# Kernel optimization log

Measured on AMD Instinct MI355X. Metric: run time of the kernel, lower is better.

Reference implementation:

```python
import jax, jax.numpy as jnp
import numpy as np

FEATURE_SIZE = 100000
FIELD_SIZE = 39
EMBED_SIZE = 16
BATCH = 4096


def setup_inputs() -> dict:
    key = jax.random.key(0)
    k1, k2, k3, k4 = jax.random.split(key, 4)
    feature_idx = jax.random.randint(k1, (BATCH, FIELD_SIZE), 0, FEATURE_SIZE)
    feature_values = jax.random.uniform(k2, (BATCH, FIELD_SIZE), dtype=jnp.float32)
    feature_embeddings = jax.random.normal(
        k3, (FEATURE_SIZE, FIELD_SIZE, EMBED_SIZE), dtype=jnp.float32)
    weights_first_order = jax.random.normal(k4, (FEATURE_SIZE, 1), dtype=jnp.float32)
    fm_bias = jnp.zeros((1,), dtype=jnp.float32)
    return {
        "feature_idx": feature_idx,
        "feature_values": feature_values,
        "feature_embeddings": feature_embeddings,
        "weights_first_order": weights_first_order,
        "fm_bias": fm_bias,
    }


def reference(feature_idx, feature_values, feature_embeddings, weights_first_order, fm_bias):
    # First order: gather per-feature scalar weights -> [B, F]
    w1 = weights_first_order[feature_idx, 0]
    first_order = jnp.sum(feature_values * w1, axis=1, keepdims=True)  # [B,1]

    # Field-aware gather: E[b, i, f, :] = feature_embeddings[idx[b,i], f, :]
    E = feature_embeddings[feature_idx]  # [B, F, F, E]

    # S[b,i,j] = <v_{i,fj}, v_{j,fi}>  (dot over embedding dim)
    S = jnp.einsum('bije,bjie->bij', E, E)  # [B, F, F]

    vv = feature_values[:, :, None] * feature_values[:, None, :]  # [B, F, F]
    F = feature_idx.shape[1]
    upper = jnp.triu(jnp.ones((F, F), dtype=bool), k=1)  # i < j pairs
    second_order = jnp.sum(jnp.where(upper, S * vv, 0.0), axis=(1, 2))[:, None]  # [B,1]

    return second_order + first_order + fm_bias
```

## Files before the change

kernel.cpp:

```cpp
#include <hip/hip_runtime.h>
#include <hip/hip_fp16.h>

#define BATCH 4096
#define FIELD 39
#define EMBED 16
#define ROW_F4 (FIELD * EMBED / 4)
#define TOT_F4 (FIELD * ROW_F4)
#define NPAIRS (FIELD * (FIELD - 1))
#define NTASKS (NPAIRS * 4)
#define BLOCK 512
#define NWAVES (BLOCK / 64)

__global__ __launch_bounds__(BLOCK) void ffm_kernel(
    const int*   __restrict__ idx,
    const float* __restrict__ vals,
    const float* __restrict__ emb,
    const float* __restrict__ w1,
    const float* __restrict__ bias,
    float*       __restrict__ out)
{
    const int b   = blockIdx.x;
    const int tid = threadIdx.x;

    __shared__ __half s_emb[FIELD * FIELD * EMBED];
    __shared__ int    s_idx[FIELD];
    __shared__ float  s_val[FIELD];
    __shared__ float  s_red[NWAVES];

    if (tid < FIELD) {
        s_idx[tid] = idx[b * FIELD + tid];
        s_val[tid] = vals[b * FIELD + tid];
    }
    __syncthreads();

    const float4* emb4 = (const float4*)emb;
    __half2* s2 = (__half2*)s_emb;
    for (int t = tid; t < TOT_F4; t += BLOCK) {
        int i   = t / ROW_F4;
        int off = t - i * ROW_F4;
        float4 g = emb4[s_idx[i] * ROW_F4 + off];
        s2[t * 2]     = __floats2half2_rn(g.x, g.y);
        s2[t * 2 + 1] = __floats2half2_rn(g.z, g.w);
    }

    float acc = 0.0f;
    if (tid < FIELD) {
        acc += s_val[tid] * w1[s_idx[tid]];
    }
    __syncthreads();

    const int e = tid & 3;
    for (int t = tid; t < NTASKS; t += BLOCK) {
        int p = t >> 2;
        int i = p / (FIELD - 1);
        int r = p - i * (FIELD - 1);
        int j = r + (r >= i ? 1 : 0);
        const __half2* a2 = (const __half2*)&s_emb[(i * FIELD + j) * EMBED + e * 4];
        const __half2* c2 = (const __half2*)&s_emb[(j * FIELD + i) * EMBED + e * 4];
        float2 a0 = __half22float2(a2[0]);
        float2 a1 = __half22float2(a2[1]);
        float2 c0 = __half22float2(c2[0]);
        float2 c1 = __half22float2(c2[1]);
        float dot = a0.x * c0.x + a0.y * c0.y + a1.x * c1.x + a1.y * c1.y;
        acc += dot * (0.5f * s_val[i] * s_val[j]);
    }

    #pragma unroll
    for (int off = 32; off > 0; off >>= 1)
        acc += __shfl_down(acc, off, 64);

    const int wave = tid >> 6;
    const int lane = tid & 63;
    if (lane == 0) s_red[wave] = acc;
    __syncthreads();

    if (tid == 0) {
        float s = 0.0f;
        #pragma unroll
        for (int w = 0; w < NWAVES; ++w) s += s_red[w];
        out[b] = s + bias[0];
    }
}

extern "C" void kernel_launch(void* const* d_in, const int* in_sizes, int n_in,
                              void* d_out, int out_size, void* d_ws, size_t ws_size,
                              hipStream_t stream) {
    const int*   idx  = (const int*)d_in[0];
    const float* vals = (const float*)d_in[1];
    const float* emb  = (const float*)d_in[2];
    const float* w1   = (const float*)d_in[3];
    const float* bias = (const float*)d_in[4];
    float* out = (float*)d_out;

    ffm_kernel<<<BATCH, BLOCK, 0, stream>>>(idx, vals, emb, w1, bias, out);
}
```

Before: 356.6 us.

## Batch global embedding loads into registers, widen LDS reads, enlarge block

Raises the block size to 1024 threads and splits the gather into two phases: every global float4 load is issued into a register array first, then converted to half and written to shared memory. This puts more loads in flight per thread. The pairwise dot products now use two threads per pair with 16-byte shared-memory reads instead of four threads with 8-byte reads, which roughly halves the LDS instruction count. The cost is higher register pressure from the unrolled load buffer, and launch bounds that ask for 8 blocks of 1024 threads, which may not be achievable.

```diff
diff --git a/kernel.cpp b/kernel.cpp
--- a/kernel.cpp
+++ b/kernel.cpp
@@ -7,11 +7,13 @@
 #define ROW_F4 (FIELD * EMBED / 4)
 #define TOT_F4 (FIELD * ROW_F4)
 #define NPAIRS (FIELD * (FIELD - 1))
-#define NTASKS (NPAIRS * 4)
-#define BLOCK 512
+#define NTASK2 (NPAIRS * 2)
+#define BLOCK 1024
 #define NWAVES (BLOCK / 64)
+#define SITER ((TOT_F4 + BLOCK - 1) / BLOCK)
+#define CITER ((NTASK2 + BLOCK - 1) / BLOCK)
 
-__global__ __launch_bounds__(BLOCK) void ffm_kernel(
+__global__ __launch_bounds__(BLOCK, 8) void ffm_kernel(
     const int*   __restrict__ idx,
     const float* __restrict__ vals,
     const float* __restrict__ emb,
@@ -22,7 +24,7 @@
     const int b   = blockIdx.x;
     const int tid = threadIdx.x;
 
-    __shared__ __half s_emb[FIELD * FIELD * EMBED];
+    __shared__ __align__(16) __half s_emb[FIELD * FIELD * EMBED];
     __shared__ int    s_idx[FIELD];
     __shared__ float  s_val[FIELD];
     __shared__ float  s_red[NWAVES];
@@ -34,35 +36,54 @@
     __syncthreads();
 
     const float4* emb4 = (const float4*)emb;
-    __half2* s2 = (__half2*)s_emb;
-    for (int t = tid; t < TOT_F4; t += BLOCK) {
-        int i   = t / ROW_F4;
-        int off = t - i * ROW_F4;
-        float4 g = emb4[s_idx[i] * ROW_F4 + off];
-        s2[t * 2]     = __floats2half2_rn(g.x, g.y);
-        s2[t * 2 + 1] = __floats2half2_rn(g.z, g.w);
+    float4 g[SITER];
+    #pragma unroll
+    for (int it = 0; it < SITER; ++it) {
+        int t  = tid + it * BLOCK;
+        int tc = t < TOT_F4 ? t : TOT_F4 - 1;
+        int i  = tc / ROW_F4;
+        int off = tc - i * ROW_F4;
+        g[it] = emb4[s_idx[i] * ROW_F4 + off];
     }
 
     float acc = 0.0f;
     if (tid < FIELD) {
-        acc += s_val[tid] * w1[s_idx[tid]];
+        acc = s_val[tid] * w1[s_idx[tid]];
+    }
+
+    __half2* s2 = (__half2*)s_emb;
+    #pragma unroll
+    for (int it = 0; it < SITER; ++it) {
+        int t = tid + it * BLOCK;
+        if (t < TOT_F4) {
+            s2[t * 2]     = __floats2half2_rn(g[it].x, g[it].y);
+            s2[t * 2 + 1] = __floats2half2_rn(g[it].z, g[it].w);
+        }
     }
     __syncthreads();
 
-    const int e = tid & 3;
-    for (int t = tid; t < NTASKS; t += BLOCK) {
-        int p = t >> 2;
-        int i = p / (FIELD - 1);
-        int r = p - i * (FIELD - 1);
-        int j = r + (r >= i ? 1 : 0);
-        const __half2* a2 = (const __half2*)&s_emb[(i * FIELD + j) * EMBED + e * 4];
-        const __half2* c2 = (const __half2*)&s_emb[(j * FIELD + i) * EMBED + e * 4];
-        float2 a0 = __half22float2(a2[0]);
-        float2 a1 = __half22float2(a2[1]);
-        float2 c0 = __half22float2(c2[0]);
-        float2 c1 = __half22float2(c2[1]);
-        float dot = a0.x * c0.x + a0.y * c0.y + a1.x * c1.x + a1.y * c1.y;
-        acc += dot * (0.5f * s_val[i] * s_val[j]);
+    #pragma unroll
+    for (int it = 0; it < CITER; ++it) {
+        int t = tid + it * BLOCK;
+        if (t < NTASK2) {
+            int p = t >> 1;
+            int h = t & 1;
+            int i = p / (FIELD - 1);
+            int r = p - i * (FIELD - 1);
+            int j = r + (r >= i ? 1 : 0);
+            float4 av = *(const float4*)&s_emb[(i * FIELD + j) * EMBED + h * 8];
+            float4 cv = *(const float4*)&s_emb[(j * FIELD + i) * EMBED + h * 8];
+            const __half2* ah = (const __half2*)&av;
+            const __half2* ch = (const __half2*)&cv;
+            float dot = 0.0f;
+            #pragma unroll
+            for (int k = 0; k < 4; ++k) {
+                float2 a = __half22float2(ah[k]);
+                float2 c = __half22float2(ch[k]);
+                dot += a.x * c.x + a.y * c.y;
+            }
+            acc += dot * (0.5f * s_val[i] * s_val[j]);
+        }
     }
 
     #pragma unroll
```

Result: faster. 344.6 us (-3.4%).
